# Kernel optimization log

Measured on AMD Instinct MI355X. Metric: run time of the kernel, lower is better.

## Reference

```python
import jax, jax.numpy as jnp
import numpy as np

B, S, D, H = 4, 2048, 1024, 16
DH = D // H  # depth per head


def setup_inputs() -> dict:
    key = jax.random.key(0)
    ks = jax.random.split(key, 12)
    s = 1.0 / np.sqrt(D)
    return {
        "v": jax.random.normal(ks[0], (B, S, D), jnp.float32),
        "k": jax.random.normal(ks[1], (B, S, D), jnp.float32),
        "q": jax.random.normal(ks[2], (B, S, D), jnp.float32),
        "mask": jnp.ones((B, 1, S, S), jnp.float32),
        "wq_w": jax.random.normal(ks[3], (D, D), jnp.float32) * s,
        "wq_b": jnp.zeros((D,), jnp.float32),
        "wk_w": jax.random.normal(ks[4], (D, D), jnp.float32) * s,
        "wk_b": jnp.zeros((D,), jnp.float32),
        "wv_w": jax.random.normal(ks[5], (D, D), jnp.float32) * s,
        "wv_b": jnp.zeros((D,), jnp.float32),
        "wo_w": jax.random.normal(ks[6], (D, D), jnp.float32) * s,
        "wo_b": jnp.zeros((D,), jnp.float32),
    }


def _split_heads(x):
    # [B, S, D] -> [B, H, S, DH]
    b, s, _ = x.shape
    return x.reshape(b, s, H, DH).transpose(0, 2, 1, 3)


def reference(v, k, q, mask, wq_w, wq_b, wk_w, wk_b, wv_w, wv_b, wo_w, wo_b):
    qh = _split_heads(q @ wq_w + wq_b)
    kh = _split_heads(k @ wk_w + wk_b)
    vh = _split_heads(v @ wv_w + wv_b)
    # scaled dot-product attention with multiplicative custom mask
    logits = jnp.einsum("bhqd,bhkd->bhqk", qh, kh) / jnp.sqrt(jnp.float32(DH))
    logits = logits * mask - 1e6 * (1.0 - mask)
    attn_weights = jax.nn.softmax(logits, axis=-1)
    ctx = jnp.einsum("bhqk,bhkd->bhqd", attn_weights, vh)
    concat = ctx.transpose(0, 2, 1, 3).reshape(-1, q.shape[1], D)
    out = concat @ wo_w + wo_b
    return out, attn_weights
```

## Files before the change

kernel.cpp:

```cpp
#include <hip/hip_runtime.h>


typedef unsigned short u16;
typedef unsigned int   u32;
typedef u16   u16x4  __attribute__((ext_vector_type(4)));
typedef u16   u16x8  __attribute__((ext_vector_type(8)));
typedef int   i32x4  __attribute__((ext_vector_type(4)));
typedef float f32x4  __attribute__((ext_vector_type(4)));
typedef __bf16 bf16x8 __attribute__((ext_vector_type(8)));

#define GLDS16(gp, lp)                                                         \
  __builtin_amdgcn_global_load_lds(                                            \
      (const __attribute__((address_space(1))) void*)(gp),                     \
      (__attribute__((address_space(3))) void*)(lp), 16, 0, 0)

__device__ __forceinline__ u16 f2bf(float x) {
  __bf16 h = (__bf16)x;
  union { __bf16 h; u16 u; } c; c.h = h; return c.u;
}

static const int Bn = 4, Sn = 2048, Dn = 1024, Hn = 16, DHn = 64;
#define MASK_NEG (-1442695.0f)

__global__ __launch_bounds__(256) void cast3_k(const float* __restrict__ q,
                                               const float* __restrict__ k,
                                               const float* __restrict__ v,
                                               u16* __restrict__ out) {
  int which = blockIdx.x >> 12;
  size_t li = (size_t)(blockIdx.x & 4095) * 256 + threadIdx.x;
  const float* src = which == 0 ? q : which == 1 ? k : v;
  const f32x4* p = (const f32x4*)src + li * 2;
  f32x4 a = p[0], b = p[1];
  u16x8 r;
  r[0]=f2bf(a[0]); r[1]=f2bf(a[1]); r[2]=f2bf(a[2]); r[3]=f2bf(a[3]);
  r[4]=f2bf(b[0]); r[5]=f2bf(b[1]); r[6]=f2bf(b[2]); r[7]=f2bf(b[3]);
  *((u16x8*)(out + (size_t)which * 8388608) + li) = r;
}

__global__ __launch_bounds__(256) void castWT4_k(const float* __restrict__ w0,
                                                 const float* __restrict__ w1,
                                                 const float* __restrict__ w2,
                                                 const float* __restrict__ w3,
                                                 u16* __restrict__ WTb) {
  __shared__ u16 tile[64][72];
  int z = blockIdx.z;
  const float* W = z == 0 ? w0 : z == 1 ? w1 : z == 2 ? w2 : w3;
  u16* WT = WTb + (size_t)z * 1048576;
  int bx = blockIdx.x, by = blockIdx.y, t = threadIdx.x;
  for (int rr = 0; rr < 4; rr++) {
    int r = rr * 16 + (t >> 4);
    int c = (t & 15) * 4;
    float4 v = *(const float4*)(W + (size_t)(by * 64 + r) * 1024 + bx * 64 + c);
    tile[c + 0][r] = f2bf(v.x); tile[c + 1][r] = f2bf(v.y);
    tile[c + 2][r] = f2bf(v.z); tile[c + 3][r] = f2bf(v.w);
  }
  __syncthreads();
  for (int rr = 0; rr < 2; rr++) {
    int gid = rr * 256 + t;
    int r = gid >> 3, g = gid & 7;
    u16x8 v = *(const u16x8*)&tile[r][g * 8];
    *(u16x8*)(WT + (size_t)(bx * 64 + r) * 1024 + by * 64 + g * 8) = v;
  }
}

__global__ __launch_bounds__(256) void flags_k(const float* __restrict__ mask,
                                               int* __restrict__ flags) {
  __shared__ int ok_s;
  int t = threadIdx.x;
  if (t == 0) ok_s = 1;
  __syncthreads();
  int qt = blockIdx.x, kt = blockIdx.y, b = blockIdx.z;
  const float* base = mask + ((size_t)b * Sn + qt * 128) * Sn + kt * 64;
  int r = t >> 1, c0 = (t & 1) * 32;
  const float* p = base + (size_t)r * Sn + c0;
  bool ok = true;
  for (int i = 0; i < 8; i++) {
    float4 v = *(const float4*)(p + i * 4);
    ok = ok && (v.x == 1.0f) && (v.y == 1.0f) && (v.z == 1.0f) && (v.w == 1.0f);
  }
  if (!ok) atomicAnd(&ok_s, 0);
  __syncthreads();
  if (t == 0) flags[(b * 32 + kt) * 16 + qt] = ok_s;
}

__device__ __forceinline__ void gemm_body(const u16* __restrict__ A,
                                          const u16* __restrict__ BT,
                                          const float* __restrict__ bias,
                                          void* __restrict__ outp, int mode,
                                          int nt, int mt, char* sm) {
  const int K = 1024;
  int m0 = mt * 128, n0 = nt * 128;
  int tid = threadIdx.x, w = tid >> 6, l = tid & 63, l15 = l & 15, l4 = l >> 4;
  int wm = w >> 1, wn = w & 1;

  size_t goff_a[4], goff_b[4];
  int lbase[4];
  for (int i = 0; i < 4; i++) {
    int gi = (w * 4 + i) * 64 + l;
    int row = gi >> 3, g = gi & 7;
    int gx = g ^ (row & 7);
    goff_a[i] = (size_t)(m0 + row) * K + gx * 8;
    goff_b[i] = (size_t)(n0 + row) * K + gx * 8;
    lbase[i] = (w * 4 + i) * 1024;
  }

  f32x4 acc[4][4] = {};
  for (int t = 0; t < 16; t++) {
    int k0 = t * 64;
    for (int i = 0; i < 4; i++) {
      GLDS16(A + goff_a[i] + k0, sm + lbase[i]);
      GLDS16(BT + goff_b[i] + k0, sm + 16384 + lbase[i]);
    }
    __syncthreads();
#pragma unroll
    for (int kk = 0; kk < 2; kk++) {
      int kb = kk * 64 + l4 * 16;
      bf16x8 af[4], bf[4];
#pragma unroll
      for (int mi = 0; mi < 4; mi++) {
        int row = wm * 64 + mi * 16 + l15;
        af[mi] = *(const bf16x8*)(sm + row * 128 + (kb ^ ((row & 7) << 4)));
      }
#pragma unroll
      for (int nj = 0; nj < 4; nj++) {
        int row = wn * 64 + nj * 16 + l15;
        bf[nj] = *(const bf16x8*)(sm + 16384 + row * 128 + (kb ^ ((row & 7) << 4)));
      }
#pragma unroll
      for (int mi = 0; mi < 4; mi++)
#pragma unroll
        for (int nj = 0; nj < 4; nj++)
          acc[mi][nj] = __builtin_amdgcn_mfma_f32_16x16x32_bf16(af[mi], bf[nj], acc[mi][nj], 0, 0, 0);
    }
    __syncthreads();
  }

  if (mode == 3) {
    float* out = (float*)outp;
#pragma unroll
    for (int mi = 0; mi < 4; mi++)
#pragma unroll
      for (int nj = 0; nj < 4; nj++)
#pragma unroll
        for (int r = 0; r < 4; r++) {
          int mg = m0 + wm * 64 + mi * 16 + l4 * 4 + r;
          int ng = n0 + wn * 64 + nj * 16 + l15;
          out[(size_t)mg * 1024 + ng] = acc[mi][nj][r] + bias[ng];
        }
  } else if (mode == 2) {
    u16* vt = (u16*)outp;
#pragma unroll
    for (int mi = 0; mi < 4; mi++)
#pragma unroll
      for (int nj = 0; nj < 4; nj++) {
        int ng = n0 + wn * 64 + nj * 16 + l15;
        int h = ng >> 6, d = ng & 63;
        int mgb = m0 + wm * 64 + mi * 16 + l4 * 4;
        int b = mgb >> 11, s = mgb & 2047;
        float bs = bias[ng];
        u16x4 pk;
#pragma unroll
        for (int r = 0; r < 4; r++) pk[r] = f2bf(acc[mi][nj][r] + bs);
        *(u16x4*)(vt + ((size_t)(b * Hn + h) * DHn + d) * Sn + s) = pk;
      }
  } else {
    u16* oh = (u16*)outp;
    float sc = (mode == 0) ? 0.18033688f : 1.0f;
#pragma unroll
    for (int mi = 0; mi < 4; mi++)
#pragma unroll
      for (int nj = 0; nj < 4; nj++) {
        int ng = n0 + wn * 64 + nj * 16 + l15;
        int h = ng >> 6, d = ng & 63;
        float bs = bias[ng];
#pragma unroll
        for (int r = 0; r < 4; r++) {
          int mg = m0 + wm * 64 + mi * 16 + l4 * 4 + r;
          int b = mg >> 11, s = mg & 2047;
          oh[((size_t)(b * Hn + h) * Sn + s) * DHn + d] = f2bf((acc[mi][nj][r] + bs) * sc);
        }
      }
  }
}

__global__ __launch_bounds__(256) void gemmO_k(const u16* __restrict__ A,
                                               const u16* __restrict__ BT,
                                               const float* __restrict__ bias,
                                               float* __restrict__ outp) {
  __shared__ __align__(16) char sm[32768];
  int hw = blockIdx.x;
  int lg = (hw & 7) * 64 + (hw >> 3);
  int nt = lg & 7, mt = lg >> 3;
  gemm_body(A, BT, bias, (void*)outp, 3, nt, mt, sm);
}

__global__ __launch_bounds__(256) void gemm3_k(const u16* __restrict__ Ab,
                                               const u16* __restrict__ BTb,
                                               const float* __restrict__ b0,
                                               const float* __restrict__ b1,
                                               const float* __restrict__ b2,
                                               u16* __restrict__ outb) {
  __shared__ __align__(16) char sm[32768];
  int hw = blockIdx.x;
  int lg = (hw & 7) * 192 + (hw >> 3);
  int z = lg >> 9, r = lg & 511;
  int nt = r & 7, mt = r >> 3;
  const u16* A = Ab + (size_t)z * 8388608;
  const u16* BT = BTb + (size_t)z * 1048576;
  const float* bias = z == 0 ? b0 : z == 1 ? b1 : b2;
  u16* out = outb + (size_t)z * 8388608;
  gemm_body(A, BT, bias, (void*)out, z, nt, mt, sm);
}

__global__ __launch_bounds__(256) void pass1_k(
    const u16* __restrict__ qh, const u16* __restrict__ kh,
    const float* __restrict__ mask, const int* __restrict__ flags,
    float* __restrict__ cvec) {
  __shared__ __align__(16) char sm[32768];
  int hw = blockIdx.x;
  int lg = (hw & 7) * 128 + (hw >> 3);
  int qt = lg & 15, h = (lg >> 4) & 15, b = lg >> 8;
  int bh = b * Hn + h;
  int tid = threadIdx.x, w = tid >> 6, l = tid & 63, l15 = l & 15, l4 = l >> 4;

  const u16* Qg = qh + ((size_t)bh * Sn + qt * 128) * DHn;
  const u16* Kg = kh + (size_t)bh * Sn * DHn;
  const float* Mg = mask + (size_t)b * Sn * Sn + (size_t)(qt * 128) * Sn;

  u32 fl = (u32)__ballot(l < 32 && flags[(b * 32 + l) * 16 + qt] != 0);

  int srow[4], sgx8[4], sdst[4];
  for (int i = 0; i < 4; i++) {
    int gid = i * 256 + tid, row = gid >> 3, g = gid & 7;
    srow[i] = row; sgx8[i] = (g ^ (row & 7)) * 8; sdst[i] = gid * 16;
  }
#define STAGE_K128(t, buf)                                                     \
  for (int i = 0; i < 4; i++)                                                  \
    GLDS16(Kg + (size_t)((t) * 128 + srow[i]) * DHn + sgx8[i], sm + (buf) + sdst[i]);

  bf16x8 qf[2][2];
#pragma unroll
  for (int ni = 0; ni < 2; ni++)
#pragma unroll
    for (int kk = 0; kk < 2; kk++)
      qf[ni][kk] = *(const bf16x8*)(Qg + (size_t)(w * 32 + ni * 16 + l15) * DHn + kk * 32 + l4 * 8);

  float lsum[2] = {0.f, 0.f};

  STAGE_K128(0, 0);
  for (int t = 0; t < 16; t++) {
    int kcur = (t & 1) ? 16384 : 0;
    __syncthreads();
    if (t < 15) { int knxt = (t & 1) ? 0 : 16384; STAGE_K128(t + 1, knxt); }
#pragma unroll
    for (int h2 = 0; h2 < 2; h2++) {
      int kt = t * 2 + h2;
      f32x4 s[4][2] = {};
#pragma unroll
      for (int kk = 0; kk < 2; kk++) {
        int kb = kk * 64 + l4 * 16;
        bf16x8 a[4];
#pragma unroll
        for (int mi = 0; mi < 4; mi++) {
          int row = h2 * 64 + mi * 16 + l15;
          a[mi] = *(const bf16x8*)(sm + kcur + row * 128 + (kb ^ ((row & 7) << 4)));
        }
#pragma unroll
        for (int mi = 0; mi < 4; mi++)
#pragma unroll
          for (int ni = 0; ni < 2; ni++)
            s[mi][ni] = __builtin_amdgcn_mfma_f32_16x16x32_bf16(a[mi], qf[ni][kk], s[mi][ni], 0, 0, 0);
      }
      if (!((fl >> kt) & 1)) {
#pragma unroll
        for (int ni = 0; ni < 2; ni++) {
          const float* mrow = Mg + (size_t)(w * 32 + ni * 16 + l15) * Sn + kt * 64;
#pragma unroll
          for (int mi = 0; mi < 4; mi++) {
            f32x4 mv = *(const f32x4*)(mrow + mi * 16 + l4 * 4);
#pragma unroll
            for (int r = 0; r < 4; r++)
              s[mi][ni][r] = s[mi][ni][r] * mv[r] + MASK_NEG * (1.f - mv[r]);
          }
        }
      }
#pragma unroll
      for (int ni = 0; ni < 2; ni++)
#pragma unroll
        for (int mi = 0; mi < 4; mi++)
#pragma unroll
          for (int r = 0; r < 4; r++) lsum[ni] += __builtin_exp2f(s[mi][ni][r]);
    }
  }
#pragma unroll
  for (int ni = 0; ni < 2; ni++) {
    lsum[ni] += __shfl_xor(lsum[ni], 16);
    lsum[ni] += __shfl_xor(lsum[ni], 32);
  }
  if (l4 == 0) {
#pragma unroll
    for (int ni = 0; ni < 2; ni++)
      cvec[(size_t)bh * Sn + qt * 128 + w * 32 + ni * 16 + l15] = __builtin_log2f(lsum[ni]);
  }
}

#define K0_OFF 0
#define K1_OFF 8192
#define V0_OFF 16384
#define V1_OFF 24576
#define P_OFF  32768

__global__ __launch_bounds__(256) void pass2_k(
    const u16* __restrict__ qh, const u16* __restrict__ kh,
    const u16* __restrict__ vt, const float* __restrict__ mask,
    const int* __restrict__ flags, const float* __restrict__ cvec,
    float* __restrict__ attn, u16* __restrict__ ctxc) {
  __shared__ __align__(16) char sm[49152];
  int hw = blockIdx.x;
  int lg = (hw & 7) * 128 + (hw >> 3);
  int qt = lg & 15, h = (lg >> 4) & 15, b = lg >> 8;
  int bh = b * Hn + h;
  int tid = threadIdx.x, w = tid >> 6, l = tid & 63, l15 = l & 15, l4 = l >> 4;

  const u16* Qg = qh + ((size_t)bh * Sn + qt * 128) * DHn;
  const u16* Kg = kh + (size_t)bh * Sn * DHn;
  const u16* Vg = vt + (size_t)bh * DHn * Sn;
  const float* Mg = mask + (size_t)b * Sn * Sn + (size_t)(qt * 128) * Sn;

  u32 fl = (u32)__ballot(l < 32 && flags[(b * 32 + l) * 16 + qt] != 0);

  float cv[2];
#pragma unroll
  for (int ni = 0; ni < 2; ni++)
    cv[ni] = cvec[(size_t)bh * Sn + qt * 128 + w * 32 + ni * 16 + l15];

  int srow[2], sgx8[2], sdst[2];
  for (int i = 0; i < 2; i++) {
    int gid = i * 256 + tid, row = gid >> 3, g = gid & 7;
    srow[i] = row; sgx8[i] = (g ^ (row & 7)) * 8; sdst[i] = gid * 16;
  }
#define STAGE_K(t, buf)                                                        \
  for (int i = 0; i < 2; i++)                                                  \
    GLDS16(Kg + (size_t)((t) * 64 + srow[i]) * DHn + sgx8[i], sm + (buf) + sdst[i]);
#define STAGE_V(t, buf)                                                        \
  for (int i = 0; i < 2; i++)                                                  \
    GLDS16(Vg + (size_t)srow[i] * Sn + (t) * 64 + sgx8[i], sm + (buf) + sdst[i]);

  bf16x8 qf[2][2];
#pragma unroll
  for (int ni = 0; ni < 2; ni++)
#pragma unroll
    for (int kk = 0; kk < 2; kk++)
      qf[ni][kk] = *(const bf16x8*)(Qg + (size_t)(w * 32 + ni * 16 + l15) * DHn + kk * 32 + l4 * 8);

  f32x4 ctx[4][2] = {};
  STAGE_K(0, K0_OFF);
  STAGE_V(0, V0_OFF);
  for (int t = 0; t < 32; t++) {
    int kcur = (t & 1) ? K1_OFF : K0_OFF;
    int vcur = (t & 1) ? V1_OFF : V0_OFF;
    __syncthreads();
    if (t < 31) {
      int knxt = (t & 1) ? K0_OFF : K1_OFF;
      int vnxt = (t & 1) ? V0_OFF : V1_OFF;
      STAGE_K(t + 1, knxt);
      STAGE_V(t + 1, vnxt);
    }
    f32x4 s[4][2] = {};
#pragma unroll
    for (int kk = 0; kk < 2; kk++) {
      int kb = kk * 64 + l4 * 16;
      bf16x8 a[4];
#pragma unroll
      for (int mi = 0; mi < 4; mi++) {
        int row = mi * 16 + l15;
        a[mi] = *(const bf16x8*)(sm + kcur + row * 128 + (kb ^ ((row & 7) << 4)));
      }
#pragma unroll
      for (int mi = 0; mi < 4; mi++)
#pragma unroll
        for (int ni = 0; ni < 2; ni++)
          s[mi][ni] = __builtin_amdgcn_mfma_f32_16x16x32_bf16(a[mi], qf[ni][kk], s[mi][ni], 0, 0, 0);
    }
    if (!((fl >> t) & 1)) {
#pragma unroll
      for (int ni = 0; ni < 2; ni++) {
        const float* mrow = Mg + (size_t)(w * 32 + ni * 16 + l15) * Sn + t * 64;
#pragma unroll
        for (int mi = 0; mi < 4; mi++) {
          f32x4 mv = *(const f32x4*)(mrow + mi * 16 + l4 * 4);
#pragma unroll
          for (int r = 0; r < 4; r++)
            s[mi][ni][r] = s[mi][ni][r] * mv[r] + MASK_NEG * (1.f - mv[r]);
        }
      }
    }
#pragma unroll
    for (int ni = 0; ni < 2; ni++)
#pragma unroll
      for (int mi = 0; mi < 4; mi++)
#pragma unroll
        for (int r = 0; r < 4; r++) s[mi][ni][r] = __builtin_exp2f(s[mi][ni][r] - cv[ni]);
#pragma unroll
    for (int ni = 0; ni < 2; ni++) {
      float* arow = attn + ((size_t)bh * Sn + qt * 128 + w * 32 + ni * 16 + l15) * Sn + t * 64;
#pragma unroll
      for (int mi = 0; mi < 4; mi++)
        *(f32x4*)(arow + mi * 16 + l4 * 4) = s[mi][ni];
    }
#pragma unroll
    for (int ni = 0; ni < 2; ni++) {
      int q = w * 32 + ni * 16 + l15;
#pragma unroll
      for (int mi = 0; mi < 4; mi++) {
        u16x4 pk;
#pragma unroll
        for (int r = 0; r < 4; r++) pk[r] = f2bf(s[mi][ni][r]);
        int kb = mi * 32 + l4 * 8;
        *(u16x4*)(sm + P_OFF + q * 128 + (kb ^ ((q & 7) << 4))) = pk;
      }
    }
#pragma unroll
    for (int kk = 0; kk < 2; kk++) {
      int kb = kk * 64 + l4 * 16;
      bf16x8 av[4], bp[2];
#pragma unroll
      for (int mi = 0; mi < 4; mi++) {
        int row = mi * 16 + l15;
        av[mi] = *(const bf16x8*)(sm + vcur + row * 128 + (kb ^ ((row & 7) << 4)));
      }
#pragma unroll
      for (int ni = 0; ni < 2; ni++) {
        int q = w * 32 + ni * 16 + l15;
        bp[ni] = *(const bf16x8*)(sm + P_OFF + q * 128 + (kb ^ ((q & 7) << 4)));
      }
#pragma unroll
      for (int mi = 0; mi < 4; mi++)
#pragma unroll
        for (int ni = 0; ni < 2; ni++)
          ctx[mi][ni] = __builtin_amdgcn_mfma_f32_16x16x32_bf16(av[mi], bp[ni], ctx[mi][ni], 0, 0, 0);
    }
  }

#pragma unroll
  for (int ni = 0; ni < 2; ni++) {
    int q = w * 32 + ni * 16 + l15;
#pragma unroll
    for (int mi = 0; mi < 4; mi++) {
      u16x4 ck;
#pragma unroll
      for (int r = 0; r < 4; r++) ck[r] = f2bf(ctx[mi][ni][r]);
      int db = mi * 32 + l4 * 8;
      *(u16x4*)(sm + P_OFF + q * 128 + (db ^ ((q & 7) << 4))) = ck;
    }
  }
  __syncthreads();
  {
    int q = tid >> 1, hf = tid & 1;
    u16* dst = ctxc + ((size_t)b * Sn + qt * 128 + q) * Dn + h * DHn + hf * 32;
#pragma unroll
    for (int c4 = 0; c4 < 4; c4++) {
      int db = hf * 64 + c4 * 16;
      i32x4 v = *(const i32x4*)(sm + P_OFF + q * 128 + (db ^ ((q & 7) << 4)));
      *(i32x4*)(dst + c4 * 8) = v;
    }
  }
}

extern "C" void kernel_launch(void* const* d_in, const int* in_sizes, int n_in,
                              void* d_out, int out_size, void* d_ws, size_t ws_size,
                              hipStream_t stream) {
  const float* v_f  = (const float*)d_in[0];
  const float* k_f  = (const float*)d_in[1];
  const float* q_f  = (const float*)d_in[2];
  const float* mask = (const float*)d_in[3];
  const float* wq_w = (const float*)d_in[4];
  const float* wq_b = (const float*)d_in[5];
  const float* wk_w = (const float*)d_in[6];
  const float* wk_b = (const float*)d_in[7];
  const float* wv_w = (const float*)d_in[8];
  const float* wv_b = (const float*)d_in[9];
  const float* wo_w = (const float*)d_in[10];
  const float* wo_b = (const float*)d_in[11];

  char* ws = (char*)d_ws;
  u16*   qbf  = (u16*)(ws + 0);
  u16*   wT   = (u16*)(ws + 50331648);
  u16*   woT  = (u16*)(ws + 56623104);
  u16*   qhp  = (u16*)(ws + 58720256);
  u16*   khp  = (u16*)(ws + 75497472);
  u16*   vtp  = (u16*)(ws + 92274688);
  u16*   ctxc = (u16*)(ws + 109051904);
  float* cvec = (float*)(ws + 125829120);
  int*   flg  = (int*)(ws + 126353408);

  float* out  = (float*)d_out;
  float* attn = out + (size_t)Bn * Sn * Dn;

  cast3_k<<<12288, 256, 0, stream>>>(q_f, k_f, v_f, qbf);
  castWT4_k<<<dim3(16, 16, 4), 256, 0, stream>>>(wq_w, wk_w, wv_w, wo_w, wT);
  flags_k<<<dim3(16, 32, 4), 256, 0, stream>>>(mask, flg);

  gemm3_k<<<1536, 256, 0, stream>>>(qbf, wT, wq_b, wk_b, wv_b, qhp);

  pass1_k<<<1024, 256, 0, stream>>>(qhp, khp, mask, flg, cvec);
  pass2_k<<<1024, 256, 0, stream>>>(qhp, khp, vtp, mask, flg, cvec, attn, ctxc);

  gemmO_k<<<512, 256, 0, stream>>>(ctxc, woT, wo_b, out);
}
```

Before: 651.5 us.

## Fuse softmax statistics pass into attention kernel, merge prep kernels, use nontemporal stores

```diff
diff --git a/kernel.cpp b/kernel.cpp
--- a/kernel.cpp
+++ b/kernel.cpp
@@ -18,69 +18,69 @@
   __bf16 h = (__bf16)x;
   union { __bf16 h; u16 u; } c; c.h = h; return c.u;
 }
+__device__ __forceinline__ void nt_store4(float* p, f32x4 v) {
+  __builtin_nontemporal_store(v, (f32x4*)p);
+}
 
 static const int Bn = 4, Sn = 2048, Dn = 1024, Hn = 16, DHn = 64;
 #define MASK_NEG (-1442695.0f)
 
-__global__ __launch_bounds__(256) void cast3_k(const float* __restrict__ q,
-                                               const float* __restrict__ k,
-                                               const float* __restrict__ v,
-                                               u16* __restrict__ out) {
-  int which = blockIdx.x >> 12;
-  size_t li = (size_t)(blockIdx.x & 4095) * 256 + threadIdx.x;
-  const float* src = which == 0 ? q : which == 1 ? k : v;
-  const f32x4* p = (const f32x4*)src + li * 2;
-  f32x4 a = p[0], b = p[1];
-  u16x8 r;
-  r[0]=f2bf(a[0]); r[1]=f2bf(a[1]); r[2]=f2bf(a[2]); r[3]=f2bf(a[3]);
-  r[4]=f2bf(b[0]); r[5]=f2bf(b[1]); r[6]=f2bf(b[2]); r[7]=f2bf(b[3]);
-  *((u16x8*)(out + (size_t)which * 8388608) + li) = r;
-}
-
-__global__ __launch_bounds__(256) void castWT4_k(const float* __restrict__ w0,
-                                                 const float* __restrict__ w1,
-                                                 const float* __restrict__ w2,
-                                                 const float* __restrict__ w3,
-                                                 u16* __restrict__ WTb) {
-  __shared__ u16 tile[64][72];
-  int z = blockIdx.z;
-  const float* W = z == 0 ? w0 : z == 1 ? w1 : z == 2 ? w2 : w3;
-  u16* WT = WTb + (size_t)z * 1048576;
-  int bx = blockIdx.x, by = blockIdx.y, t = threadIdx.x;
-  for (int rr = 0; rr < 4; rr++) {
-    int r = rr * 16 + (t >> 4);
-    int c = (t & 15) * 4;
-    float4 v = *(const float4*)(W + (size_t)(by * 64 + r) * 1024 + bx * 64 + c);
-    tile[c + 0][r] = f2bf(v.x); tile[c + 1][r] = f2bf(v.y);
-    tile[c + 2][r] = f2bf(v.z); tile[c + 3][r] = f2bf(v.w);
-  }
-  __syncthreads();
-  for (int rr = 0; rr < 2; rr++) {
-    int gid = rr * 256 + t;
-    int r = gid >> 3, g = gid & 7;
-    u16x8 v = *(const u16x8*)&tile[r][g * 8];
-    *(u16x8*)(WT + (size_t)(bx * 64 + r) * 1024 + by * 64 + g * 8) = v;
-  }
-}
-
-__global__ __launch_bounds__(256) void flags_k(const float* __restrict__ mask,
-                                               int* __restrict__ flags) {
+__global__ __launch_bounds__(256) void prep_k(
+    const float* __restrict__ q, const float* __restrict__ k,
+    const float* __restrict__ v, const float* __restrict__ mask,
+    const float* __restrict__ w0, const float* __restrict__ w1,
+    const float* __restrict__ w2, const float* __restrict__ w3,
+    u16* __restrict__ qkv, u16* __restrict__ WTb, int* __restrict__ flags) {
+  __shared__ __align__(16) u16 tile[64][72];
   __shared__ int ok_s;
-  int t = threadIdx.x;
-  if (t == 0) ok_s = 1;
-  __syncthreads();
-  int qt = blockIdx.x, kt = blockIdx.y, b = blockIdx.z;
-  const float* base = mask + ((size_t)b * Sn + qt * 128) * Sn + kt * 64;
-  int r = t >> 1, c0 = (t & 1) * 32;
-  const float* p = base + (size_t)r * Sn + c0;
-  bool ok = true;
-  for (int i = 0; i < 8; i++) {
-    float4 v = *(const float4*)(p + i * 4);
-    ok = ok && (v.x == 1.0f) && (v.y == 1.0f) && (v.z == 1.0f) && (v.w == 1.0f);
-  }
-  if (!ok) atomicAnd(&ok_s, 0);
-  __syncthreads();
-  if (t == 0) flags[(b * 32 + kt) * 16 + qt] = ok_s;
+  int bid = blockIdx.x, t = threadIdx.x;
+
+  if (bid < 12288) {
+    int which = bid >> 12;
+    size_t li = (size_t)(bid & 4095) * 256 + t;
+    const float* src = which == 0 ? q : which == 1 ? k : v;
+    const f32x4* p = (const f32x4*)src + li * 2;
+    f32x4 a = p[0], b = p[1];
+    u16x8 r;
+    r[0]=f2bf(a[0]); r[1]=f2bf(a[1]); r[2]=f2bf(a[2]); r[3]=f2bf(a[3]);
+    r[4]=f2bf(b[0]); r[5]=f2bf(b[1]); r[6]=f2bf(b[2]); r[7]=f2bf(b[3]);
+    *((u16x8*)(qkv + (size_t)which * 8388608) + li) = r;
+  } else if (bid < 13312) {
+    int i = bid - 12288;
+    int z = i >> 8, rem = i & 255, bx = rem & 15, by = rem >> 4;
+    const float* W = z == 0 ? w0 : z == 1 ? w1 : z == 2 ? w2 : w3;
+    u16* WT = WTb + (size_t)z * 1048576;
+    for (int rr = 0; rr < 4; rr++) {
+      int r = rr * 16 + (t >> 4);
+      int c = (t & 15) * 4;
+      float4 vv = *(const float4*)(W + (size_t)(by * 64 + r) * 1024 + bx * 64 + c);
+      tile[c + 0][r] = f2bf(vv.x); tile[c + 1][r] = f2bf(vv.y);
+      tile[c + 2][r] = f2bf(vv.z); tile[c + 3][r] = f2bf(vv.w);
+    }
+    __syncthreads();
+    for (int rr = 0; rr < 2; rr++) {
+      int gid = rr * 256 + t;
+      int r = gid >> 3, g = gid & 7;
+      u16x8 vv = *(const u16x8*)&tile[r][g * 8];
+      *(u16x8*)(WT + (size_t)(bx * 64 + r) * 1024 + by * 64 + g * 8) = vv;
+    }
+  } else {
+    int i = bid - 13312;
+    int qt = i & 15, kt = (i >> 4) & 31, b = i >> 9;
+    if (t == 0) ok_s = 1;
+    __syncthreads();
+    const float* base = mask + ((size_t)b * Sn + qt * 128) * Sn + kt * 64;
+    int r = t >> 1, c0 = (t & 1) * 32;
+    const float* p = base + (size_t)r * Sn + c0;
+    bool ok = true;
+    for (int j = 0; j < 8; j++) {
+      float4 vv = *(const float4*)(p + j * 4);
+      ok = ok && (vv.x == 1.0f) && (vv.y == 1.0f) && (vv.z == 1.0f) && (vv.w == 1.0f);
+    }
+    if (!ok) atomicAnd(&ok_s, 0);
+    __syncthreads();
+    if (t == 0) flags[(b * 32 + kt) * 16 + qt] = ok_s;
+  }
 }
 
 __device__ __forceinline__ void gemm_body(const u16* __restrict__ A,
@@ -145,7 +145,8 @@
         for (int r = 0; r < 4; r++) {
           int mg = m0 + wm * 64 + mi * 16 + l4 * 4 + r;
           int ng = n0 + wn * 64 + nj * 16 + l15;
-          out[(size_t)mg * 1024 + ng] = acc[mi][nj][r] + bias[ng];
+          __builtin_nontemporal_store(acc[mi][nj][r] + bias[ng],
+                                      out + (size_t)mg * 1024 + ng);
         }
   } else if (mode == 2) {
     u16* vt = (u16*)outp;
@@ -212,109 +213,17 @@
   gemm_body(A, BT, bias, (void*)out, z, nt, mt, sm);
 }
 
-__global__ __launch_bounds__(256) void pass1_k(
-    const u16* __restrict__ qh, const u16* __restrict__ kh,
-    const float* __restrict__ mask, const int* __restrict__ flags,
-    float* __restrict__ cvec) {
-  __shared__ __align__(16) char sm[32768];
-  int hw = blockIdx.x;
-  int lg = (hw & 7) * 128 + (hw >> 3);
-  int qt = lg & 15, h = (lg >> 4) & 15, b = lg >> 8;
-  int bh = b * Hn + h;
-  int tid = threadIdx.x, w = tid >> 6, l = tid & 63, l15 = l & 15, l4 = l >> 4;
-
-  const u16* Qg = qh + ((size_t)bh * Sn + qt * 128) * DHn;
-  const u16* Kg = kh + (size_t)bh * Sn * DHn;
-  const float* Mg = mask + (size_t)b * Sn * Sn + (size_t)(qt * 128) * Sn;
-
-  u32 fl = (u32)__ballot(l < 32 && flags[(b * 32 + l) * 16 + qt] != 0);
-
-  int srow[4], sgx8[4], sdst[4];
-  for (int i = 0; i < 4; i++) {
-    int gid = i * 256 + tid, row = gid >> 3, g = gid & 7;
-    srow[i] = row; sgx8[i] = (g ^ (row & 7)) * 8; sdst[i] = gid * 16;
-  }
-#define STAGE_K128(t, buf)                                                     \
-  for (int i = 0; i < 4; i++)                                                  \
-    GLDS16(Kg + (size_t)((t) * 128 + srow[i]) * DHn + sgx8[i], sm + (buf) + sdst[i]);
-
-  bf16x8 qf[2][2];
-#pragma unroll
-  for (int ni = 0; ni < 2; ni++)
-#pragma unroll
-    for (int kk = 0; kk < 2; kk++)
-      qf[ni][kk] = *(const bf16x8*)(Qg + (size_t)(w * 32 + ni * 16 + l15) * DHn + kk * 32 + l4 * 8);
-
-  float lsum[2] = {0.f, 0.f};
-
-  STAGE_K128(0, 0);
-  for (int t = 0; t < 16; t++) {
-    int kcur = (t & 1) ? 16384 : 0;
-    __syncthreads();
-    if (t < 15) { int knxt = (t & 1) ? 0 : 16384; STAGE_K128(t + 1, knxt); }
-#pragma unroll
-    for (int h2 = 0; h2 < 2; h2++) {
-      int kt = t * 2 + h2;
-      f32x4 s[4][2] = {};
-#pragma unroll
-      for (int kk = 0; kk < 2; kk++) {
-        int kb = kk * 64 + l4 * 16;
-        bf16x8 a[4];
-#pragma unroll
-        for (int mi = 0; mi < 4; mi++) {
-          int row = h2 * 64 + mi * 16 + l15;
-          a[mi] = *(const bf16x8*)(sm + kcur + row * 128 + (kb ^ ((row & 7) << 4)));
-        }
-#pragma unroll
-        for (int mi = 0; mi < 4; mi++)
-#pragma unroll
-          for (int ni = 0; ni < 2; ni++)
-            s[mi][ni] = __builtin_amdgcn_mfma_f32_16x16x32_bf16(a[mi], qf[ni][kk], s[mi][ni], 0, 0, 0);
-      }
-      if (!((fl >> kt) & 1)) {
-#pragma unroll
-        for (int ni = 0; ni < 2; ni++) {
-          const float* mrow = Mg + (size_t)(w * 32 + ni * 16 + l15) * Sn + kt * 64;
-#pragma unroll
-          for (int mi = 0; mi < 4; mi++) {
-            f32x4 mv = *(const f32x4*)(mrow + mi * 16 + l4 * 4);
-#pragma unroll
-            for (int r = 0; r < 4; r++)
-              s[mi][ni][r] = s[mi][ni][r] * mv[r] + MASK_NEG * (1.f - mv[r]);
-          }
-        }
-      }
-#pragma unroll
-      for (int ni = 0; ni < 2; ni++)
-#pragma unroll
-        for (int mi = 0; mi < 4; mi++)
-#pragma unroll
-          for (int r = 0; r < 4; r++) lsum[ni] += __builtin_exp2f(s[mi][ni][r]);
-    }
-  }
-#pragma unroll
-  for (int ni = 0; ni < 2; ni++) {
-    lsum[ni] += __shfl_xor(lsum[ni], 16);
-    lsum[ni] += __shfl_xor(lsum[ni], 32);
-  }
-  if (l4 == 0) {
-#pragma unroll
-    for (int ni = 0; ni < 2; ni++)
-      cvec[(size_t)bh * Sn + qt * 128 + w * 32 + ni * 16 + l15] = __builtin_log2f(lsum[ni]);
-  }
-}
-
 #define K0_OFF 0
 #define K1_OFF 8192
 #define V0_OFF 16384
 #define V1_OFF 24576
 #define P_OFF  32768
 
-__global__ __launch_bounds__(256) void pass2_k(
+__global__ __launch_bounds__(256) void attn_k(
     const u16* __restrict__ qh, const u16* __restrict__ kh,
     const u16* __restrict__ vt, const float* __restrict__ mask,
-    const int* __restrict__ flags, const float* __restrict__ cvec,
-    float* __restrict__ attn, u16* __restrict__ ctxc) {
+    const int* __restrict__ flags, float* __restrict__ attn,
+    u16* __restrict__ ctxc) {
   __shared__ __align__(16) char sm[49152];
   int hw = blockIdx.x;
   int lg = (hw & 7) * 128 + (hw >> 3);
@@ -329,22 +238,20 @@
 
   u32 fl = (u32)__ballot(l < 32 && flags[(b * 32 + l) * 16 + qt] != 0);
 
-  float cv[2];
-#pragma unroll
-  for (int ni = 0; ni < 2; ni++)
-    cv[ni] = cvec[(size_t)bh * Sn + qt * 128 + w * 32 + ni * 16 + l15];
-
-  int srow[2], sgx8[2], sdst[2];
-  for (int i = 0; i < 2; i++) {
+  int srowA[4], sgxA[4], sdstA[4];
+  for (int i = 0; i < 4; i++) {
     int gid = i * 256 + tid, row = gid >> 3, g = gid & 7;
-    srow[i] = row; sgx8[i] = (g ^ (row & 7)) * 8; sdst[i] = gid * 16;
-  }
+    srowA[i] = row; sgxA[i] = (g ^ (row & 7)) * 8; sdstA[i] = gid * 16;
+  }
+#define STAGE_KA(t, buf)                                                       \
+  for (int i = 0; i < 4; i++)                                                  \
+    GLDS16(Kg + (size_t)((t) * 128 + srowA[i]) * DHn + sgxA[i], sm + (buf) + sdstA[i]);
 #define STAGE_K(t, buf)                                                        \
   for (int i = 0; i < 2; i++)                                                  \
-    GLDS16(Kg + (size_t)((t) * 64 + srow[i]) * DHn + sgx8[i], sm + (buf) + sdst[i]);
+    GLDS16(Kg + (size_t)((t) * 64 + srowA[i]) * DHn + sgxA[i], sm + (buf) + sdstA[i]);
 #define STAGE_V(t, buf)                                                        \
   for (int i = 0; i < 2; i++)                                                  \
-    GLDS16(Vg + (size_t)srow[i] * Sn + (t) * 64 + sgx8[i], sm + (buf) + sdst[i]);
+    GLDS16(Vg + (size_t)srowA[i] * Sn + (t) * 64 + sgxA[i], sm + (buf) + sdstA[i]);
 
   bf16x8 qf[2][2];
 #pragma unroll
@@ -353,6 +260,61 @@
     for (int kk = 0; kk < 2; kk++)
       qf[ni][kk] = *(const bf16x8*)(Qg + (size_t)(w * 32 + ni * 16 + l15) * DHn + kk * 32 + l4 * 8);
 
+  float lsum[2] = {0.f, 0.f};
+  STAGE_KA(0, 0);
+  for (int t = 0; t < 16; t++) {
+    int kcur = (t & 1) ? 16384 : 0;
+    __syncthreads();
+    if (t < 15) { int knxt = (t & 1) ? 0 : 16384; STAGE_KA(t + 1, knxt); }
+#pragma unroll
+    for (int h2 = 0; h2 < 2; h2++) {
+      int kt = t * 2 + h2;
+      f32x4 s[4][2] = {};
+#pragma unroll
+      for (int kk = 0; kk < 2; kk++) {
+        int kb = kk * 64 + l4 * 16;
+        bf16x8 a[4];
+#pragma unroll
+        for (int mi = 0; mi < 4; mi++) {
+          int row = h2 * 64 + mi * 16 + l15;
+          a[mi] = *(const bf16x8*)(sm + kcur + row * 128 + (kb ^ ((row & 7) << 4)));
+        }
+#pragma unroll
+        for (int mi = 0; mi < 4; mi++)
+#pragma unroll
+          for (int ni = 0; ni < 2; ni++)
+            s[mi][ni] = __builtin_amdgcn_mfma_f32_16x16x32_bf16(a[mi], qf[ni][kk], s[mi][ni], 0, 0, 0);
+      }
+      if (!((fl >> kt) & 1)) {
+#pragma unroll
+        for (int ni = 0; ni < 2; ni++) {
+          const float* mrow = Mg + (size_t)(w * 32 + ni * 16 + l15) * Sn + kt * 64;
+#pragma unroll
+          for (int mi = 0; mi < 4; mi++) {
+            f32x4 mv = *(const f32x4*)(mrow + mi * 16 + l4 * 4);
+#pragma unroll
+            for (int r = 0; r < 4; r++)
+              s[mi][ni][r] = s[mi][ni][r] * mv[r] + MASK_NEG * (1.f - mv[r]);
+          }
+        }
+      }
+#pragma unroll
+      for (int ni = 0; ni < 2; ni++)
+#pragma unroll
+        for (int mi = 0; mi < 4; mi++)
+#pragma unroll
+          for (int r = 0; r < 4; r++) lsum[ni] += __builtin_exp2f(s[mi][ni][r]);
+    }
+  }
+  float cv[2];
+#pragma unroll
+  for (int ni = 0; ni < 2; ni++) {
+    lsum[ni] += __shfl_xor(lsum[ni], 16);
+    lsum[ni] += __shfl_xor(lsum[ni], 32);
+    cv[ni] = __builtin_log2f(lsum[ni]);
+  }
+
+  __syncthreads();
   f32x4 ctx[4][2] = {};
   STAGE_K(0, K0_OFF);
   STAGE_V(0, V0_OFF);
@@ -406,7 +368,7 @@
       float* arow = attn + ((size_t)bh * Sn + qt * 128 + w * 32 + ni * 16 + l15) * Sn + t * 64;
 #pragma unroll
       for (int mi = 0; mi < 4; mi++)
-        *(f32x4*)(arow + mi * 16 + l4 * 4) = s[mi][ni];
+        nt_store4(arow + mi * 16 + l4 * 4, s[mi][ni]);
     }
 #pragma unroll
     for (int ni = 0; ni < 2; ni++) {
@@ -491,20 +453,14 @@
   u16*   khp  = (u16*)(ws + 75497472);
   u16*   vtp  = (u16*)(ws + 92274688);
   u16*   ctxc = (u16*)(ws + 109051904);
-  float* cvec = (float*)(ws + 125829120);
-  int*   flg  = (int*)(ws + 126353408);
+  int*   flg  = (int*)(ws + 125829120);
 
   float* out  = (float*)d_out;
   float* attn = out + (size_t)Bn * Sn * Dn;
 
-  cast3_k<<<12288, 256, 0, stream>>>(q_f, k_f, v_f, qbf);
-  castWT4_k<<<dim3(16, 16, 4), 256, 0, stream>>>(wq_w, wk_w, wv_w, wo_w, wT);
-  flags_k<<<dim3(16, 32, 4), 256, 0, stream>>>(mask, flg);
-
+  prep_k<<<15360, 256, 0, stream>>>(q_f, k_f, v_f, mask,
+                                    wq_w, wk_w, wv_w, wo_w, qbf, wT, flg);
   gemm3_k<<<1536, 256, 0, stream>>>(qbf, wT, wq_b, wk_b, wv_b, qhp);
-
-  pass1_k<<<1024, 256, 0, stream>>>(qhp, khp, mask, flg, cvec);
-  pass2_k<<<1024, 256, 0, stream>>>(qhp, khp, vtp, mask, flg, cvec, attn, ctxc);
-
+  attn_k<<<1024, 256, 0, stream>>>(qhp, khp, vtp, mask, flg, attn, ctxc);
   gemmO_k<<<512, 256, 0, stream>>>(ctxc, woT, wo_b, out);
 }
```

Result: faster. 564.9 us (-13.3%).
